# Kernel optimization log

Hardware: AMD Instinct MI355X
Metric: run time of the kernel (lower is better)

The kernel has to match this reference:

```python
import jax, jax.numpy as jnp
import numpy as np

IMG_SIZE = 1024
B, G, A, N = 64, 128, 3, 1280
COORD_L, OBJ_L, NOOBJ_L = 5.0, 1.0, 0.5


def setup_inputs() -> dict:
    key = jax.random.key(0)
    k1, k2, k3, k4 = jax.random.split(key, 4)
    y_pred = jax.random.normal(k1, (B, G, G, A * 5), dtype=jnp.float32)
    # ground boxes in pixel coords: centers in [0, IMG_SIZE), w/h in [8, 208)
    xy = jax.random.uniform(k2, (N, 2), dtype=jnp.float32) * (IMG_SIZE - 1e-3)
    wh = jax.random.uniform(k3, (N, 2), dtype=jnp.float32) * 200.0 + 8.0
    ground_bboxes = jnp.concatenate([xy, wh], axis=1)
    anchors = jnp.array([[10.0, 13.0], [16.0, 30.0], [33.0, 23.0]], dtype=jnp.float32)
    batch_idx = jnp.sort(jax.random.randint(k4, (N,), 0, B))
    return {"y_pred": y_pred, "ground_bboxes": ground_bboxes, "anchors": anchors, "batch_idx": batch_idx}


def _build_target(ground_bboxes, anchors, batch_idx, stride, dtype):
    sa = anchors / stride                      # [A,2] scaled anchors
    gb = ground_bboxes / stride                # [N,4] grid-space boxes
    gx, gy, gw, gh = gb[:, 0], gb[:, 1], gb[:, 2], gb[:, 3]
    gi = gx.astype(jnp.int32)                  # grid col
    gj = gy.astype(jnp.int32)                  # grid row
    # wh-IoU of every gt box vs every anchor: [N,A]
    inter = jnp.minimum(sa[None, :, 0], gw[:, None]) * jnp.minimum(sa[None, :, 1], gh[:, None])
    union = sa[None, :, 0] * sa[None, :, 1] + (gw * gh)[:, None] - inter
    best = jnp.argmax(inter / union, axis=1)   # [N] best anchor per gt
    aw, ah = sa[best, 0], sa[best, 1]
    vals = jnp.stack([jnp.ones_like(gx),       # t_conf = 1
                      gx - gi, gy - gj,        # tx, ty
                      jnp.log(gw / aw), jnp.log(gh / ah)], axis=-1)  # tw, th
    tgt = jnp.zeros((B, A, G, G, 5), dtype).at[batch_idx, best, gj, gi].set(vals)
    return tgt[..., 0], tgt[..., 1], tgt[..., 2], tgt[..., 3], tgt[..., 4]


def reference(y_pred, ground_bboxes, anchors, batch_idx):
    stride = IMG_SIZE / G
    # [B,G,G,A,5] -> [B,A,G,G,5]
    pred = y_pred.reshape(B, G, G, A, 5).transpose(0, 3, 1, 2, 4)
    conf_logit = pred[..., 0]
    x = jax.nn.sigmoid(pred[..., 1])
    y = jax.nn.sigmoid(pred[..., 2])
    w = pred[..., 3]
    h = pred[..., 4]
    t_conf, tx, ty, tw, th = _build_target(ground_bboxes, anchors, batch_idx, stride, y_pred.dtype)
    m = t_conf                                  # 1.0 at object cells, else 0
    loss_coord = COORD_L * jnp.sum(m * ((x - tx) ** 2 + (y - ty) ** 2 + (w - tw) ** 2 + (h - th) ** 2))
    # BCE(sigmoid(z), 1) = -log_sigmoid(z); BCE(sigmoid(z), 0) = -log_sigmoid(-z)
    loss_obj = OBJ_L * jnp.sum(-m * jax.nn.log_sigmoid(conf_logit))
    loss_noobj = NOOBJ_L * jnp.sum(-(1.0 - m) * jax.nn.log_sigmoid(-conf_logit))
    return loss_coord + loss_obj + loss_noobj
```

## Files before the change

kernel.cpp:

```cpp
#include <hip/hip_runtime.h>
#include <math.h>

#define NBOX   1280
#define BVAL   64
#define GVAL   128
#define NFLOAT (BVAL * GVAL * GVAL * 15)
#define NVEC   (NFLOAT / 4)

__device__ __forceinline__ float softplus_f(float z) {
    return fmaxf(z, 0.f) + __logf(1.f + __expf(-fabsf(z)));
}

__global__ void __launch_bounds__(256) yolo_loss_kernel(
    const float* __restrict__ yp,
    const float* __restrict__ gbox,
    const float* __restrict__ anch,
    const int*   __restrict__ bidx,
    float*       __restrict__ out)
{
    __shared__ int   skey[NBOX];
    __shared__ int   sb[NBOX];
    __shared__ float sv[NBOX][4];
    __shared__ float swave[4];

    const int t = threadIdx.x;
    float acc = 0.f;

    if (blockIdx.x == 0) {
        for (int n = t; n < NBOX; n += 256) {
            float gx = gbox[n * 4 + 0] * 0.125f;
            float gy = gbox[n * 4 + 1] * 0.125f;
            float gw = gbox[n * 4 + 2] * 0.125f;
            float gh = gbox[n * 4 + 3] * 0.125f;
            int gi = (int)gx, gj = (int)gy;
            int best = 0; float bestr = -1.f, baw = 1.f, bah = 1.f;
            #pragma unroll
            for (int a = 0; a < 3; a++) {
                float aw = anch[a * 2 + 0] * 0.125f;
                float ah = anch[a * 2 + 1] * 0.125f;
                float inter = fminf(aw, gw) * fminf(ah, gh);
                float uni   = aw * ah + gw * gh - inter;
                float r     = inter / uni;
                if (r > bestr) { bestr = r; best = a; baw = aw; bah = ah; }
            }
            int b = bidx[n];
            skey[n]  = ((b * 3 + best) * 128 + gj) * 128 + gi;
            sb[n]    = b;
            sv[n][0] = gx - (float)gi;
            sv[n][1] = gy - (float)gj;
            sv[n][2] = __logf(gw / baw);
            sv[n][3] = __logf(gh / bah);
        }
        __syncthreads();
        for (int n = t; n < NBOX; n += 256) {
            int key = skey[n], b = sb[n];
            bool winner = true;
            for (int m2 = n + 1; m2 < NBOX; m2++) {
                if (sb[m2] != b) break;
                if (skey[m2] == key) { winner = false; break; }
            }
            if (winner) {
                int gi = key & 127;
                int gj = (key >> 7) & 127;
                int ba = key >> 14;
                int best = ba % 3;
                int b2   = ba / 3;
                long base = ((((long)b2 * GVAL + gj) * GVAL) + gi) * 15 + best * 5;
                float conf = yp[base + 0];
                float px = 1.f / (1.f + __expf(-yp[base + 1]));
                float py = 1.f / (1.f + __expf(-yp[base + 2]));
                float pw = yp[base + 3];
                float ph = yp[base + 4];
                float dx = px - sv[n][0];
                float dy = py - sv[n][1];
                float dw = pw - sv[n][2];
                float dh = ph - sv[n][3];
                float lp = __logf(1.f + __expf(-fabsf(conf)));
                float sp_pos = fmaxf( conf, 0.f) + lp;
                float sp_neg = fmaxf(-conf, 0.f) + lp;
                acc += 5.f * (dx * dx + dy * dy + dw * dw + dh * dh)
                     + sp_neg - 0.5f * sp_pos;
            }
        }
    } else {
        const float4* yp4 = (const float4*)yp;
        int idx    = (blockIdx.x - 1) * 256 + t;
        int stride = (gridDim.x - 1) * 256;
        float lacc = 0.f;
        for (int v = idx; v < NVEC; v += stride) {
            float4 d = yp4[v];
            int r = (v * 4) % 15;
            float vals[4] = {d.x, d.y, d.z, d.w};
            #pragma unroll
            for (int k = 0; k < 4; k++) {
                int rr = r + k; if (rr >= 15) rr -= 15;
                if ((0x421u >> rr) & 1u)
                    lacc += softplus_f(vals[k]);
            }
        }
        acc = 0.5f * lacc;
    }

    #pragma unroll
    for (int off = 32; off > 0; off >>= 1) acc += __shfl_down(acc, off, 64);
    int lane = t & 63, wid = t >> 6;
    if (lane == 0) swave[wid] = acc;
    __syncthreads();
    if (t == 0) {
        float s = swave[0] + swave[1] + swave[2] + swave[3];
        atomicAdd(out, s);
    }
}

extern "C" void kernel_launch(void* const* d_in, const int* in_sizes, int n_in,
                              void* d_out, int out_size, void* d_ws, size_t ws_size,
                              hipStream_t stream) {
    const float* yp   = (const float*)d_in[0];
    const float* gbox = (const float*)d_in[1];
    const float* anch = (const float*)d_in[2];
    const int*   bidx = (const int*)d_in[3];
    float* out = (float*)d_out;

    hipMemsetAsync(out, 0, sizeof(float), stream);

    yolo_loss_kernel<<<dim3(2048), dim3(256), 0, stream>>>(yp, gbox, anch, bidx, out);
}
```

Baseline: 123.1 us.

## Stage prediction tiles through LDS so each thread handles one cell's conf logits

The streaming blocks now copy 960-float4 tiles (256 cells × 15 floats) into shared memory with coalesced loads, then each thread reads the three conf logits of one cell. This removes the per-element modulo/mask logic and the wasted softplus branches. The price is two barriers per tile and strided LDS reads that may hit bank conflicts. To fit the tile, block 0 no longer keeps per-box targets in shared memory and recomputes them from global memory for winning boxes, and the grid grows by one block.

```diff
diff --git a/kernel.cpp b/kernel.cpp
--- a/kernel.cpp
+++ b/kernel.cpp
@@ -1,11 +1,14 @@
 #include <hip/hip_runtime.h>
 #include <math.h>
 
-#define NBOX   1280
-#define BVAL   64
-#define GVAL   128
-#define NFLOAT (BVAL * GVAL * GVAL * 15)
-#define NVEC   (NFLOAT / 4)
+#define NBOX     1280
+#define BVAL     64
+#define GVAL     128
+#define NFLOAT   (BVAL * GVAL * GVAL * 15)
+#define NVEC     (NFLOAT / 4)
+#define TILE_V4  960
+#define TILE_F   3840
+#define NTILES   (NVEC / TILE_V4)
 
 __device__ __forceinline__ float softplus_f(float z) {
     return fmaxf(z, 0.f) + __logf(1.f + __expf(-fabsf(z)));
@@ -18,22 +21,22 @@
     const int*   __restrict__ bidx,
     float*       __restrict__ out)
 {
-    __shared__ int   skey[NBOX];
-    __shared__ int   sb[NBOX];
-    __shared__ float sv[NBOX][4];
+    __shared__ float sm[TILE_F];
     __shared__ float swave[4];
 
     const int t = threadIdx.x;
     float acc = 0.f;
 
     if (blockIdx.x == 0) {
+        int* skey = (int*)sm;
+        int* sb   = ((int*)sm) + NBOX;
         for (int n = t; n < NBOX; n += 256) {
             float gx = gbox[n * 4 + 0] * 0.125f;
             float gy = gbox[n * 4 + 1] * 0.125f;
             float gw = gbox[n * 4 + 2] * 0.125f;
             float gh = gbox[n * 4 + 3] * 0.125f;
             int gi = (int)gx, gj = (int)gy;
-            int best = 0; float bestr = -1.f, baw = 1.f, bah = 1.f;
+            int best = 0; float bestr = -1.f;
             #pragma unroll
             for (int a = 0; a < 3; a++) {
                 float aw = anch[a * 2 + 0] * 0.125f;
@@ -41,15 +44,11 @@
                 float inter = fminf(aw, gw) * fminf(ah, gh);
                 float uni   = aw * ah + gw * gh - inter;
                 float r     = inter / uni;
-                if (r > bestr) { bestr = r; best = a; baw = aw; bah = ah; }
+                if (r > bestr) { bestr = r; best = a; }
             }
             int b = bidx[n];
-            skey[n]  = ((b * 3 + best) * 128 + gj) * 128 + gi;
-            sb[n]    = b;
-            sv[n][0] = gx - (float)gi;
-            sv[n][1] = gy - (float)gj;
-            sv[n][2] = __logf(gw / baw);
-            sv[n][3] = __logf(gh / bah);
+            skey[n] = ((b * 3 + best) * 128 + gj) * 128 + gi;
+            sb[n]   = b;
         }
         __syncthreads();
         for (int n = t; n < NBOX; n += 256) {
@@ -60,21 +59,32 @@
                 if (skey[m2] == key) { winner = false; break; }
             }
             if (winner) {
-                int gi = key & 127;
-                int gj = (key >> 7) & 127;
-                int ba = key >> 14;
-                int best = ba % 3;
-                int b2   = ba / 3;
-                long base = ((((long)b2 * GVAL + gj) * GVAL) + gi) * 15 + best * 5;
+                float gx = gbox[n * 4 + 0] * 0.125f;
+                float gy = gbox[n * 4 + 1] * 0.125f;
+                float gw = gbox[n * 4 + 2] * 0.125f;
+                float gh = gbox[n * 4 + 3] * 0.125f;
+                int gi = (int)gx, gj = (int)gy;
+                int best = 0; float bestr = -1.f, baw = 1.f, bah = 1.f;
+                #pragma unroll
+                for (int a = 0; a < 3; a++) {
+                    float aw = anch[a * 2 + 0] * 0.125f;
+                    float ah = anch[a * 2 + 1] * 0.125f;
+                    float inter = fminf(aw, gw) * fminf(ah, gh);
+                    float uni   = aw * ah + gw * gh - inter;
+                    float r     = inter / uni;
+                    if (r > bestr) { bestr = r; best = a; baw = aw; bah = ah; }
+                }
+                float tx = gx - (float)gi;
+                float ty = gy - (float)gj;
+                float tw = __logf(gw / baw);
+                float th = __logf(gh / bah);
+                long base = ((((long)b * GVAL + gj) * GVAL) + gi) * 15 + best * 5;
                 float conf = yp[base + 0];
                 float px = 1.f / (1.f + __expf(-yp[base + 1]));
                 float py = 1.f / (1.f + __expf(-yp[base + 2]));
                 float pw = yp[base + 3];
                 float ph = yp[base + 4];
-                float dx = px - sv[n][0];
-                float dy = py - sv[n][1];
-                float dw = pw - sv[n][2];
-                float dh = ph - sv[n][3];
+                float dx = px - tx, dy = py - ty, dw = pw - tw, dh = ph - th;
                 float lp = __logf(1.f + __expf(-fabsf(conf)));
                 float sp_pos = fmaxf( conf, 0.f) + lp;
                 float sp_neg = fmaxf(-conf, 0.f) + lp;
@@ -84,19 +94,18 @@
         }
     } else {
         const float4* yp4 = (const float4*)yp;
-        int idx    = (blockIdx.x - 1) * 256 + t;
-        int stride = (gridDim.x - 1) * 256;
+        float4* sm4 = (float4*)sm;
         float lacc = 0.f;
-        for (int v = idx; v < NVEC; v += stride) {
-            float4 d = yp4[v];
-            int r = (v * 4) % 15;
-            float vals[4] = {d.x, d.y, d.z, d.w};
-            #pragma unroll
-            for (int k = 0; k < 4; k++) {
-                int rr = r + k; if (rr >= 15) rr -= 15;
-                if ((0x421u >> rr) & 1u)
-                    lacc += softplus_f(vals[k]);
-            }
+        for (int tile = (int)blockIdx.x - 1; tile < NTILES; tile += (int)gridDim.x - 1) {
+            const float4* src = yp4 + (long)tile * TILE_V4;
+            sm4[t]       = src[t];
+            sm4[t + 256] = src[t + 256];
+            sm4[t + 512] = src[t + 512];
+            if (t < 192) sm4[t + 768] = src[t + 768];
+            __syncthreads();
+            int w = t * 15;
+            lacc += softplus_f(sm[w]) + softplus_f(sm[w + 5]) + softplus_f(sm[w + 10]);
+            __syncthreads();
         }
         acc = 0.5f * lacc;
     }
@@ -119,9 +128,9 @@
     const float* gbox = (const float*)d_in[1];
     const float* anch = (const float*)d_in[2];
     const int*   bidx = (const int*)d_in[3];
+
     float* out = (float*)d_out;
-
     hipMemsetAsync(out, 0, sizeof(float), stream);
 
-    yolo_loss_kernel<<<dim3(2048), dim3(256), 0, stream>>>(yp, gbox, anch, bidx, out);
+    yolo_loss_kernel<<<dim3(2049), dim3(256), 0, stream>>>(yp, gbox, anch, bidx, out);
 }
```

Result: no change. 124.9 us (+1.5%).
